# Kernel tuning notes

Measured on AMD Instinct MI355X. Metric: run time of the kernel, lower is better.

## Reference

```python
import jax, jax.numpy as jnp
import numpy as np

N_HEADS = 16

def setup_inputs() -> dict:
    key = jax.random.key(0)
    ks = jax.random.split(key, 8)
    B, S, D = 2, 2048, 1024
    s = 0.02
    return {
        "hidden_states": jax.random.normal(ks[0], (B, S, D), jnp.float32),
        "attention_mask": jnp.ones((B, S), jnp.int32),
        "script_types": jax.random.randint(ks[1], (B, S), 0, 4),
        "Wq": jax.random.normal(ks[2], (D, D), jnp.float32) * s,
        "bq": jnp.zeros((D,), jnp.float32),
        "Wk": jax.random.normal(ks[3], (D, D), jnp.float32) * s,
        "bk": jnp.zeros((D,), jnp.float32),
        "Wv": jax.random.normal(ks[4], (D, D), jnp.float32) * s,
        "bv": jnp.zeros((D,), jnp.float32),
        "Wo": jax.random.normal(ks[5], (D, D), jnp.float32) * s,
        "bo": jnp.zeros((D,), jnp.float32),
        "script_w": jnp.ones((4, N_HEADS), jnp.float32),
    }

def _heads(x, H):
    B, S, D = x.shape
    return x.reshape(B, S, H, D // H).transpose(0, 2, 1, 3)  # [B,H,S,hd]

def reference(hidden_states, attention_mask, script_types, Wq, bq, Wk, bk, Wv, bv, Wo, bo, script_w):
    B, S, D = hidden_states.shape
    H = N_HEADS
    hd = D // H
    q = _heads(hidden_states @ Wq + bq, H)
    k = _heads(hidden_states @ Wk + bk, H)
    v = _heads(hidden_states @ Wv + bv, H)
    # script-dependent per-head query scaling: [B,S,H] -> [B,H,S,1]
    sw = script_w[script_types].transpose(0, 2, 1)[..., None]
    q = q * sw
    scores = jnp.einsum("bhqd,bhkd->bhqk", q, k) / jnp.sqrt(jnp.float32(hd))
    mask = attention_mask[:, None, None, :]  # [B,1,1,S]
    scores = jnp.where(mask == 0, -jnp.inf, scores)
    probs = jax.nn.softmax(scores, axis=-1)  # dropout is identity in eval mode
    ctx = jnp.einsum("bhqk,bhkd->bhqd", probs, v)
    ctx = ctx.transpose(0, 2, 1, 3).reshape(B, S, D)
    out = ctx @ Wo + bo
    return out, probs
```

## Files before the change

### kernel.cpp

```cpp
#include <hip/hip_runtime.h>
#include <hip/hip_bf16.h>
#include <cstdint>
#include <cstddef>

typedef __attribute__((ext_vector_type(8))) short short8;
typedef __attribute__((ext_vector_type(4))) float f32x4;

#define MFMA16(a,b,c) __builtin_amdgcn_mfma_f32_16x16x32_bf16((a),(b),(c),0,0,0)
#define NEG_INF (-__builtin_inff())

__device__ __forceinline__ unsigned short f2bf(float f) {
    union { float f; unsigned int u; } a; a.f = f;
    return (unsigned short)((a.u + 0x7FFFu + ((a.u >> 16) & 1u)) >> 16);
}

__device__ __forceinline__ void gload16(const void* g, void* l) {
    __builtin_amdgcn_global_load_lds(
        (const __attribute__((address_space(1))) void*)g,
        (__attribute__((address_space(3))) void*)l, 16, 0, 0);
}

__global__ __launch_bounds__(256) void convert_bf16(const float* __restrict__ src,
                                                    unsigned short* __restrict__ dst, int n) {
    int i = (blockIdx.x * 256 + threadIdx.x) * 4;
    if (i + 3 < n) {
        float4 v = *(const float4*)(src + i);
        ushort4 o;
        o.x = f2bf(v.x); o.y = f2bf(v.y); o.z = f2bf(v.z); o.w = f2bf(v.w);
        *(ushort4*)(dst + i) = o;
    }
}

__global__ __launch_bounds__(256) void transpose_w(const float* __restrict__ W,
                                                   unsigned short* __restrict__ WT) {
    __shared__ float tile[32][33];
    int tx = threadIdx.x & 31, ty = threadIdx.x >> 5;
    int kb = blockIdx.x * 32, nb = blockIdx.y * 32;
    #pragma unroll
    for (int r = 0; r < 32; r += 8)
        tile[ty + r][tx] = W[(size_t)(kb + ty + r) * 1024 + nb + tx];
    __syncthreads();
    #pragma unroll
    for (int r = 0; r < 32; r += 8) {
        float v = tile[tx][ty + r];
        WT[(size_t)(nb + ty + r) * 1024 + kb + tx] = f2bf(v);
    }
}

__global__ __launch_bounds__(256) void pack_bias(const float* __restrict__ bq,
                                                 const float* __restrict__ bk,
                                                 const float* __restrict__ bv,
                                                 float* __restrict__ dst) {
    int i = blockIdx.x * 256 + threadIdx.x;
    if (i < 3072) {
        const float* s = (i < 1024) ? bq : (i < 2048) ? bk : bv;
        dst[i] = s[i & 1023];
    }
}

__global__ __launch_bounds__(256) void transpose_v(const unsigned short* __restrict__ V,
                                                   unsigned short* __restrict__ Vt) {
    __shared__ unsigned short tl[64][65];
    int bh = blockIdx.x >> 5;
    int kt = blockIdx.x & 31;
    int t = threadIdx.x;
    int row = t >> 2, off = (t & 3) * 16;
    const unsigned short* src = V + ((size_t)bh * 2048 + kt * 64 + row) * 64 + off;
    uint4 d0 = *(const uint4*)src;
    uint4 d1 = *(const uint4*)(src + 8);
    unsigned short tmp[16];
    *(uint4*)tmp = d0; *(uint4*)(tmp + 8) = d1;
    #pragma unroll
    for (int e = 0; e < 16; e++) tl[row][off + e] = tmp[e];
    __syncthreads();
    int d = t >> 2, ko = (t & 3) * 16;
    unsigned short o[16];
    #pragma unroll
    for (int e = 0; e < 16; e++) o[e] = tl[ko + e][d];
    unsigned short* dst = Vt + ((size_t)bh * 64 + d) * 2048 + kt * 64 + ko;
    *(uint4*)dst = *(uint4*)o;
    *(uint4*)(dst + 8) = *(uint4*)(o + 8);
}

__global__ __launch_bounds__(256) void gemm_bt(const unsigned short* __restrict__ A,
                                               const unsigned short* __restrict__ BT,
                                               const float* __restrict__ bias,
                                               unsigned short* __restrict__ qkv_out,
                                               float* __restrict__ f32_out,
                                               int mode) {
    __shared__ alignas(16) unsigned short As[4096];
    __shared__ alignas(16) unsigned short Bs[4096];
    const int t = threadIdx.x;
    const int wave = t >> 6, lane = t & 63, quad = lane >> 4, l16 = lane & 15;
    const int m0 = blockIdx.x * 128, n0 = blockIdx.y * 128;
    const int wm = (wave >> 1) * 64, wn = (wave & 1) * 64;
    const int r4 = lane >> 2, c16 = (lane & 3) << 4;
    const char* Ag = (const char*)A + (size_t)(m0 + wave * 32 + r4) * 2048 + c16;
    const char* Bg = (const char*)BT + (size_t)(n0 + wave * 32 + r4) * 2048 + c16;
    char* Al = (char*)As + wave * 2048;
    char* Bl = (char*)Bs + wave * 2048;
    f32x4 acc[4][4] = {};
    for (int k0 = 0; k0 < 1024; k0 += 32) {
        __syncthreads();
        gload16(Ag + k0 * 2, Al);
        gload16(Ag + k0 * 2 + 32768, Al + 1024);
        gload16(Bg + k0 * 2, Bl);
        gload16(Bg + k0 * 2 + 32768, Bl + 1024);
        __syncthreads();
        short8 af[4], bfr[4];
        #pragma unroll
        for (int i = 0; i < 4; i++)
            af[i] = *(const short8*)((const char*)As + (wm + i * 16 + l16) * 64 + (quad << 4));
        #pragma unroll
        for (int j = 0; j < 4; j++)
            bfr[j] = *(const short8*)((const char*)Bs + (wn + j * 16 + l16) * 64 + (quad << 4));
        #pragma unroll
        for (int i = 0; i < 4; i++)
            #pragma unroll
            for (int j = 0; j < 4; j++)
                acc[i][j] = MFMA16(af[i], bfr[j], acc[i][j]);
    }
    #pragma unroll
    for (int i = 0; i < 4; i++) {
        int tokb = m0 + wm + i * 16 + quad * 4;
        #pragma unroll
        for (int j = 0; j < 4; j++) {
            int n = n0 + wn + j * 16 + l16;
            float bv = bias[n];
            #pragma unroll
            for (int r = 0; r < 4; r++) {
                float v = acc[i][j][r] + bv;
                int tok = tokb + r;
                if (mode == 0) {
                    int which = n >> 10, n1 = n & 1023, h = n1 >> 6, d = n1 & 63;
                    int b = tok >> 11, s = tok & 2047;
                    qkv_out[(size_t)which * 4194304 + (((size_t)(b * 16 + h)) * 2048 + s) * 64 + d] = f2bf(v);
                } else {
                    f32_out[(size_t)tok * 1024 + n] = v;
                }
            }
        }
    }
}

__global__ __launch_bounds__(256, 4) void attn(const unsigned short* __restrict__ Q,
                                               const unsigned short* __restrict__ K,
                                               const unsigned short* __restrict__ Vt,
                                               const int* __restrict__ amask,
                                               const int* __restrict__ stypes,
                                               const float* __restrict__ script_w,
                                               float* __restrict__ probs,
                                               unsigned short* __restrict__ ctx) {
    __shared__ alignas(16) unsigned short Ks[2][4096];
    __shared__ alignas(16) unsigned short Vts[2][4096];
    __shared__ alignas(16) unsigned short Ps[4][16][64];
    const int t = threadIdx.x;
    const int wave = t >> 6, lane = t & 63, quad = lane >> 4, l16 = lane & 15;
    const int bid = blockIdx.y * 32 + blockIdx.x;
    const int swz = (bid & 7) * 128 + (bid >> 3);
    const int qt = swz & 31, bh = swz >> 5;
    const int b = bh >> 4, h = bh & 15;
    const int q0 = qt * 64;
    const int qrow = q0 + wave * 16 + l16;
    const int sx16 = (l16 & 7) << 4;

    const int st = stypes[b * 2048 + qrow];
    const float sfac = script_w[st * 16 + h] * 0.125f;

    const size_t qbase = ((size_t)bh * 2048 + qrow) * 64;
    const short8 aQ0 = *(const short8*)(Q + qbase + quad * 8);
    const short8 aQ1 = *(const short8*)(Q + qbase + 32 + quad * 8);

    const char* Kg = (const char*)(K + (size_t)bh * 131072);
    const char* Vg = (const char*)(Vt + (size_t)bh * 131072);
    const int* am = amask + b * 2048;

    const int r8 = lane >> 3;
    const int cx = ((lane & 7) ^ r8) << 4;

#define STAGE_K(kt_, buf_) do { \
        const char* _g = Kg + (size_t)(kt_) * 8192 + wave * 2048 + r8 * 128 + cx; \
        char* _l = (char*)&Ks[buf_][0] + wave * 2048; \
        gload16(_g, _l); gload16(_g + 1024, _l + 1024); \
    } while (0)
#define STAGE_V(kt_, buf_) do { \
        const char* _g = Vg + (size_t)(wave * 16 + r8) * 4096 + (kt_) * 128 + cx; \
        char* _l = (char*)&Vts[buf_][0] + wave * 2048; \
        gload16(_g, _l); gload16(_g + 32768, _l + 1024); \
    } while (0)

    float lsum = 0.f;
    STAGE_K(0, 0);
    __syncthreads();
    {
        int cur = 0;
        for (int kt = 0; kt < 32; kt++) {
            if (kt < 31) STAGE_K(kt + 1, cur ^ 1);
            __builtin_amdgcn_sched_barrier(0);
            f32x4 sc[4] = {};
            const char* kbl = (const char*)&Ks[cur][0];
            #pragma unroll
            for (int j = 0; j < 4; j++) {
                const char* rp = kbl + (j * 16 + l16) * 128;
                short8 bk0 = *(const short8*)(rp + ((quad << 4) ^ sx16));
                short8 bk1 = *(const short8*)(rp + ((64 + (quad << 4)) ^ sx16));
                sc[j] = MFMA16(bk0, aQ0, sc[j]);
                sc[j] = MFMA16(bk1, aQ1, sc[j]);
            }
            #pragma unroll
            for (int j = 0; j < 4; j++) {
                int4 mi = *(const int4*)(am + kt * 64 + j * 16 + quad * 4);
                lsum += __expf(fmaf(sc[j][0], sfac, mi.x ? 0.f : NEG_INF));
                lsum += __expf(fmaf(sc[j][1], sfac, mi.y ? 0.f : NEG_INF));
                lsum += __expf(fmaf(sc[j][2], sfac, mi.z ? 0.f : NEG_INF));
                lsum += __expf(fmaf(sc[j][3], sfac, mi.w ? 0.f : NEG_INF));
            }
            __syncthreads();
            cur ^= 1;
        }
    }
    lsum += __shfl_xor(lsum, 16, 64);
    lsum += __shfl_xor(lsum, 32, 64);
    const float inv_l = (lsum > 0.f) ? 1.0f / lsum : 0.0f;

    f32x4 oacc[4] = {};
    STAGE_K(0, 0);
    STAGE_V(0, 0);
    asm volatile("s_waitcnt vmcnt(0)" ::: "memory");
    __builtin_amdgcn_s_barrier();
    __builtin_amdgcn_sched_barrier(0);
    {
        int cur = 0;
        char* psrow = (char*)&Ps[wave][l16][0];
        for (int kt = 0; kt < 32; kt++) {
            if (kt < 31) { STAGE_K(kt + 1, cur ^ 1); STAGE_V(kt + 1, cur ^ 1); }
            __builtin_amdgcn_sched_barrier(0);
            f32x4 sc[4] = {};
            const char* kbl = (const char*)&Ks[cur][0];
            #pragma unroll
            for (int j = 0; j < 4; j++) {
                const char* rp = kbl + (j * 16 + l16) * 128;
                short8 bk0 = *(const short8*)(rp + ((quad << 4) ^ sx16));
                short8 bk1 = *(const short8*)(rp + ((64 + (quad << 4)) ^ sx16));
                sc[j] = MFMA16(bk0, aQ0, sc[j]);
                sc[j] = MFMA16(bk1, aQ1, sc[j]);
            }
            short8 v0[4], v1[4];
            const char* vbl = (const char*)&Vts[cur][0];
            #pragma unroll
            for (int j2 = 0; j2 < 4; j2++) {
                const char* rp = vbl + (j2 * 16 + l16) * 128;
                v0[j2] = *(const short8*)(rp + ((quad << 4) ^ sx16));
                v1[j2] = *(const short8*)(rp + ((64 + (quad << 4)) ^ sx16));
            }
            const size_t pbase = ((size_t)bh * 2048 + qrow) * 2048 + kt * 64 + quad * 4;
            #pragma unroll
            for (int j = 0; j < 4; j++) {
                int4 mi = *(const int4*)(am + kt * 64 + j * 16 + quad * 4);
                float p0 = __expf(fmaf(sc[j][0], sfac, mi.x ? 0.f : NEG_INF)) * inv_l;
                float p1 = __expf(fmaf(sc[j][1], sfac, mi.y ? 0.f : NEG_INF)) * inv_l;
                float p2 = __expf(fmaf(sc[j][2], sfac, mi.z ? 0.f : NEG_INF)) * inv_l;
                float p3 = __expf(fmaf(sc[j][3], sfac, mi.w ? 0.f : NEG_INF)) * inv_l;
                float4 pv; pv.x = p0; pv.y = p1; pv.z = p2; pv.w = p3;
                *(float4*)(probs + pbase + j * 16) = pv;
                ushort4 pq; pq.x = f2bf(p0); pq.y = f2bf(p1); pq.z = f2bf(p2); pq.w = f2bf(p3);
                *(ushort4*)(psrow + ((j * 32 + quad * 8) ^ sx16)) = pq;
            }
            asm volatile("s_waitcnt lgkmcnt(0)" ::: "memory");
            __builtin_amdgcn_sched_barrier(0);
            short8 aP0 = *(const short8*)(psrow + ((quad << 4) ^ sx16));
            short8 aP1 = *(const short8*)(psrow + ((64 + (quad << 4)) ^ sx16));
            #pragma unroll
            for (int j2 = 0; j2 < 4; j2++) oacc[j2] = MFMA16(aP0, v0[j2], oacc[j2]);
            #pragma unroll
            for (int j2 = 0; j2 < 4; j2++) oacc[j2] = MFMA16(aP1, v1[j2], oacc[j2]);
            asm volatile("s_waitcnt vmcnt(4)" ::: "memory");
            __builtin_amdgcn_s_barrier();
            __builtin_amdgcn_sched_barrier(0);
            cur ^= 1;
        }
    }
#undef STAGE_K
#undef STAGE_V
    #pragma unroll
    for (int j2 = 0; j2 < 4; j2++)
        #pragma unroll
        for (int r = 0; r < 4; r++) {
            int qr = q0 + wave * 16 + quad * 4 + r;
            ctx[((size_t)b * 2048 + qr) * 1024 + h * 64 + j2 * 16 + l16] = f2bf(oacc[j2][r]);
        }
}

extern "C" void kernel_launch(void* const* d_in, const int* in_sizes, int n_in,
                              void* d_out, int out_size, void* d_ws, size_t ws_size,
                              hipStream_t stream) {
    const float* X    = (const float*)d_in[0];
    const int*  amask = (const int*)d_in[1];
    const int*  stp   = (const int*)d_in[2];
    const float* Wq   = (const float*)d_in[3];
    const float* bq   = (const float*)d_in[4];
    const float* Wk   = (const float*)d_in[5];
    const float* bk   = (const float*)d_in[6];
    const float* Wv   = (const float*)d_in[7];
    const float* bv   = (const float*)d_in[8];
    const float* Wo   = (const float*)d_in[9];
    const float* bo   = (const float*)d_in[10];
    const float* sw   = (const float*)d_in[11];

    float* out   = (float*)d_out;
    float* probs = out + 4194304;

    char* ws = (char*)d_ws;
    unsigned short* Xb    = (unsigned short*)(ws);
    unsigned short* WqkvT = (unsigned short*)(ws + 8388608);
    unsigned short* WoT   = (unsigned short*)(ws + 14680064);
    float*          biasq = (float*)(ws + 16777216);
    unsigned short* Qb    = (unsigned short*)(ws + 16789504);
    unsigned short* Vb    = (unsigned short*)(ws + 33566720);
    unsigned short* Vtb   = (unsigned short*)(ws + 41955328);
    unsigned short* Ctx   = (unsigned short*)(ws + 50343936);
    unsigned short* Kb    = Qb + 4194304;

    convert_bf16<<<4096, 256, 0, stream>>>(X, Xb, 4194304);
    transpose_w<<<dim3(32, 32), 256, 0, stream>>>(Wq, WqkvT);
    transpose_w<<<dim3(32, 32), 256, 0, stream>>>(Wk, WqkvT + 1048576);
    transpose_w<<<dim3(32, 32), 256, 0, stream>>>(Wv, WqkvT + 2097152);
    transpose_w<<<dim3(32, 32), 256, 0, stream>>>(Wo, WoT);
    pack_bias<<<12, 256, 0, stream>>>(bq, bk, bv, biasq);
    gemm_bt<<<dim3(32, 24), 256, 0, stream>>>(Xb, WqkvT, biasq, Qb, nullptr, 0);
    transpose_v<<<1024, 256, 0, stream>>>(Vb, Vtb);
    attn<<<dim3(32, 32), 256, 0, stream>>>(Qb, Kb, Vtb, amask, stp, sw, probs, Ctx);
    gemm_bt<<<dim3(32, 8), 256, 0, stream>>>(Ctx, WoT, bo, nullptr, out, 1);
}
```

Before: 298.4 us.

## Fuse prep kernels into one launch, widen attention blocks to 128 query rows

Merges the bf16 conversion, four weight transposes and bias packing into a single prep kernel, which cuts launch count. The attention kernel now runs 512 threads (8 waves) per block over 128 query rows, so each staged K/V tile is shared by twice as many rows and K/V global traffic halves. The softmax normalization is folded into the exponent as a -log(sum) bias instead of a multiply per element. Larger blocks may lower occupancy under the launch bounds and leave fewer blocks to cover the device.

Result: no change. 304.1 us (+1.9%).

```diff
diff --git a/kernel.cpp b/kernel.cpp
--- a/kernel.cpp
+++ b/kernel.cpp
@@ -20,41 +20,48 @@
         (__attribute__((address_space(3))) void*)l, 16, 0, 0);
 }
 
-__global__ __launch_bounds__(256) void convert_bf16(const float* __restrict__ src,
-                                                    unsigned short* __restrict__ dst, int n) {
-    int i = (blockIdx.x * 256 + threadIdx.x) * 4;
-    if (i + 3 < n) {
-        float4 v = *(const float4*)(src + i);
+__global__ __launch_bounds__(256) void prep(const float* __restrict__ X,
+                                            unsigned short* __restrict__ Xb,
+                                            const float* __restrict__ Wq,
+                                            const float* __restrict__ Wk,
+                                            const float* __restrict__ Wv,
+                                            const float* __restrict__ Wo,
+                                            unsigned short* __restrict__ WqkvT,
+                                            unsigned short* __restrict__ WoT,
+                                            const float* __restrict__ bq,
+                                            const float* __restrict__ bk,
+                                            const float* __restrict__ bv,
+                                            float* __restrict__ biasq) {
+    const int bid = blockIdx.x;
+    const int t = threadIdx.x;
+    if (bid < 4096) {
+        int i = (bid * 256 + t) * 4;
+        float4 v = *(const float4*)(X + i);
         ushort4 o;
         o.x = f2bf(v.x); o.y = f2bf(v.y); o.z = f2bf(v.z); o.w = f2bf(v.w);
-        *(ushort4*)(dst + i) = o;
-    }
-}
-
-__global__ __launch_bounds__(256) void transpose_w(const float* __restrict__ W,
-                                                   unsigned short* __restrict__ WT) {
-    __shared__ float tile[32][33];
-    int tx = threadIdx.x & 31, ty = threadIdx.x >> 5;
-    int kb = blockIdx.x * 32, nb = blockIdx.y * 32;
-    #pragma unroll
-    for (int r = 0; r < 32; r += 8)
-        tile[ty + r][tx] = W[(size_t)(kb + ty + r) * 1024 + nb + tx];
-    __syncthreads();
-    #pragma unroll
-    for (int r = 0; r < 32; r += 8) {
-        float v = tile[tx][ty + r];
-        WT[(size_t)(nb + ty + r) * 1024 + kb + tx] = f2bf(v);
-    }
-}
-
-__global__ __launch_bounds__(256) void pack_bias(const float* __restrict__ bq,
-                                                 const float* __restrict__ bk,
-                                                 const float* __restrict__ bv,
-                                                 float* __restrict__ dst) {
-    int i = blockIdx.x * 256 + threadIdx.x;
-    if (i < 3072) {
-        const float* s = (i < 1024) ? bq : (i < 2048) ? bk : bv;
-        dst[i] = s[i & 1023];
+        *(ushort4*)(Xb + i) = o;
+    } else if (bid < 8192) {
+        __shared__ float tile[32][33];
+        const int wid = bid - 4096;
+        const int which = wid >> 10, t32 = wid & 1023;
+        const float* W = (which == 0) ? Wq : (which == 1) ? Wk : (which == 2) ? Wv : Wo;
+        unsigned short* WT = (which < 3) ? (WqkvT + which * 1048576) : WoT;
+        int tx = t & 31, ty = t >> 5;
+        int kb = (t32 & 31) * 32, nb = (t32 >> 5) * 32;
+        #pragma unroll
+        for (int r = 0; r < 32; r += 8)
+            tile[ty + r][tx] = W[(size_t)(kb + ty + r) * 1024 + nb + tx];
+        __syncthreads();
+        #pragma unroll
+        for (int r = 0; r < 32; r += 8) {
+            float v = tile[tx][ty + r];
+            WT[(size_t)(nb + ty + r) * 1024 + kb + tx] = f2bf(v);
+        }
+    } else {
+        for (int i = t; i < 3072; i += 256) {
+            const float* s = (i < 1024) ? bq : (i < 2048) ? bk : bv;
+            biasq[i] = s[i & 1023];
+        }
     }
 }
 
@@ -143,7 +150,7 @@
     }
 }
 
-__global__ __launch_bounds__(256, 4) void attn(const unsigned short* __restrict__ Q,
+__global__ __launch_bounds__(512, 4) void attn(const unsigned short* __restrict__ Q,
                                                const unsigned short* __restrict__ K,
                                                const unsigned short* __restrict__ Vt,
                                                const int* __restrict__ amask,
@@ -153,14 +160,14 @@
                                                unsigned short* __restrict__ ctx) {
     __shared__ alignas(16) unsigned short Ks[2][4096];
     __shared__ alignas(16) unsigned short Vts[2][4096];
-    __shared__ alignas(16) unsigned short Ps[4][16][64];
+    __shared__ alignas(16) unsigned short Ps[8][16][64];
     const int t = threadIdx.x;
     const int wave = t >> 6, lane = t & 63, quad = lane >> 4, l16 = lane & 15;
-    const int bid = blockIdx.y * 32 + blockIdx.x;
-    const int swz = (bid & 7) * 128 + (bid >> 3);
-    const int qt = swz & 31, bh = swz >> 5;
+    const int bid = blockIdx.y * 16 + blockIdx.x;
+    const int swz = (bid & 7) * 64 + (bid >> 3);
+    const int qt = swz & 15, bh = swz >> 4;
     const int b = bh >> 4, h = bh & 15;
-    const int q0 = qt * 64;
+    const int q0 = qt * 128;
     const int qrow = q0 + wave * 16 + l16;
     const int sx16 = (l16 & 7) << 4;
 
@@ -178,16 +185,12 @@
     const int r8 = lane >> 3;
     const int cx = ((lane & 7) ^ r8) << 4;
 
-#define STAGE_K(kt_, buf_) do { \
-        const char* _g = Kg + (size_t)(kt_) * 8192 + wave * 2048 + r8 * 128 + cx; \
-        char* _l = (char*)&Ks[buf_][0] + wave * 2048; \
-        gload16(_g, _l); gload16(_g + 1024, _l + 1024); \
-    } while (0)
-#define STAGE_V(kt_, buf_) do { \
-        const char* _g = Vg + (size_t)(wave * 16 + r8) * 4096 + (kt_) * 128 + cx; \
-        char* _l = (char*)&Vts[buf_][0] + wave * 2048; \
-        gload16(_g, _l); gload16(_g + 32768, _l + 1024); \
-    } while (0)
+#define STAGE_K(kt_, buf_) \
+    gload16(Kg + (size_t)(kt_) * 8192 + (wave * 8 + r8) * 128 + cx, \
+            (char*)&Ks[buf_][0] + wave * 1024)
+#define STAGE_V(kt_, buf_) \
+    gload16(Vg + (size_t)(wave * 8 + r8) * 4096 + (kt_) * 128 + cx, \
+            (char*)&Vts[buf_][0] + wave * 1024)
 
     float lsum = 0.f;
     STAGE_K(0, 0);
@@ -221,7 +224,7 @@
     }
     lsum += __shfl_xor(lsum, 16, 64);
     lsum += __shfl_xor(lsum, 32, 64);
-    const float inv_l = (lsum > 0.f) ? 1.0f / lsum : 0.0f;
+    const float lbias = (lsum > 0.f) ? -__logf(lsum) : NEG_INF;
 
     f32x4 oacc[4] = {};
     STAGE_K(0, 0);
@@ -257,10 +260,10 @@
             #pragma unroll
             for (int j = 0; j < 4; j++) {
                 int4 mi = *(const int4*)(am + kt * 64 + j * 16 + quad * 4);
-                float p0 = __expf(fmaf(sc[j][0], sfac, mi.x ? 0.f : NEG_INF)) * inv_l;
-                float p1 = __expf(fmaf(sc[j][1], sfac, mi.y ? 0.f : NEG_INF)) * inv_l;
-                float p2 = __expf(fmaf(sc[j][2], sfac, mi.z ? 0.f : NEG_INF)) * inv_l;
-                float p3 = __expf(fmaf(sc[j][3], sfac, mi.w ? 0.f : NEG_INF)) * inv_l;
+                float p0 = __expf(fmaf(sc[j][0], sfac, mi.x ? lbias : NEG_INF));
+                float p1 = __expf(fmaf(sc[j][1], sfac, mi.y ? lbias : NEG_INF));
+                float p2 = __expf(fmaf(sc[j][2], sfac, mi.z ? lbias : NEG_INF));
+                float p3 = __expf(fmaf(sc[j][3], sfac, mi.w ? lbias : NEG_INF));
                 float4 pv; pv.x = p0; pv.y = p1; pv.z = p2; pv.w = p3;
                 *(float4*)(probs + pbase + j * 16) = pv;
                 ushort4 pq; pq.x = f2bf(p0); pq.y = f2bf(p1); pq.z = f2bf(p2); pq.w = f2bf(p3);
@@ -321,14 +324,9 @@
     unsigned short* Ctx   = (unsigned short*)(ws + 50343936);
     unsigned short* Kb    = Qb + 4194304;
 
-    convert_bf16<<<4096, 256, 0, stream>>>(X, Xb, 4194304);
-    transpose_w<<<dim3(32, 32), 256, 0, stream>>>(Wq, WqkvT);
-    transpose_w<<<dim3(32, 32), 256, 0, stream>>>(Wk, WqkvT + 1048576);
-    transpose_w<<<dim3(32, 32), 256, 0, stream>>>(Wv, WqkvT + 2097152);
-    transpose_w<<<dim3(32, 32), 256, 0, stream>>>(Wo, WoT);
-    pack_bias<<<12, 256, 0, stream>>>(bq, bk, bv, biasq);
+    prep<<<8193, 256, 0, stream>>>(X, Xb, Wq, Wk, Wv, Wo, WqkvT, WoT, bq, bk, bv, biasq);
     gemm_bt<<<dim3(32, 24), 256, 0, stream>>>(Xb, WqkvT, biasq, Qb, nullptr, 0);
     transpose_v<<<1024, 256, 0, stream>>>(Vb, Vtb);
-    attn<<<dim3(32, 32), 256, 0, stream>>>(Qb, Kb, Vtb, amask, stp, sw, probs, Ctx);
+    attn<<<dim3(16, 32), 512, 0, stream>>>(Qb, Kb, Vtb, amask, stp, sw, probs, Ctx);
     gemm_bt<<<dim3(32, 8), 256, 0, stream>>>(Ctx, WoT, bo, nullptr, out, 1);
 }
```
